# Kernel tuning notes

Measured on AMD Instinct MI355X. Metric: run time of the kernel, lower is better.

Reference implementation:

```python
import jax, jax.numpy as jnp
import numpy as np
import math

B, N, E, H = 2, 2048, 1024, 16
D = E // H

def setup_inputs() -> dict:
    key = jax.random.key(0)
    ks = jax.random.split(key, 9)
    s = 1.0 / math.sqrt(E)
    return {
        "x": jax.random.normal(ks[0], (B, N, E), dtype=jnp.float32),
        "Wq": jax.random.uniform(ks[1], (E, E), jnp.float32, -s, s),
        "bq": jax.random.uniform(ks[2], (E,), jnp.float32, -s, s),
        "Wk": jax.random.uniform(ks[3], (E, E), jnp.float32, -s, s),
        "bk": jax.random.uniform(ks[4], (E,), jnp.float32, -s, s),
        "Wv": jax.random.uniform(ks[5], (E, E), jnp.float32, -s, s),
        "bv": jax.random.uniform(ks[6], (E,), jnp.float32, -s, s),
        "Wo": jax.random.uniform(ks[7], (E, E), jnp.float32, -s, s),
        "bo": jax.random.uniform(ks[8], (E,), jnp.float32, -s, s),
    }

def _split_heads(t):
    # [b, n, (h d)] -> [b, h, n, d]
    b, n, _ = t.shape
    return t.reshape(b, n, H, D).transpose(0, 2, 1, 3)

def reference(x, Wq, bq, Wk, bk, Wv, bv, Wo, bo):
    q = _split_heads(x @ Wq.T + bq)
    k = _split_heads(x @ Wk.T + bk)
    v = _split_heads(x @ Wv.T + bv)
    energy = jnp.einsum('bhqd,bhkd->bhqk', q, k)
    # Faithful to source: softmax first, THEN divide by sqrt(n_embedding)
    attention = jax.nn.softmax(energy, axis=-1) / jnp.sqrt(jnp.float32(E))
    out = jnp.einsum('bhqk,bhkd->bhqd', attention, v)
    out = out.transpose(0, 2, 1, 3).reshape(x.shape[0], x.shape[1], E)
    return out @ Wo.T + bo
```

## Files before the change

kernel.cpp:

```cpp
#include <hip/hip_runtime.h>


typedef __bf16 bf16x8 __attribute__((ext_vector_type(8)));
typedef float  f32x4  __attribute__((ext_vector_type(4)));
typedef float  f32x16 __attribute__((ext_vector_type(16)));
using u16 = unsigned short;
using u32 = unsigned int;
typedef u16 u16x8 __attribute__((ext_vector_type(8)));
typedef u16 u16x4 __attribute__((ext_vector_type(4)));
typedef u32 u32x4 __attribute__((ext_vector_type(4)));

constexpr int BATCH = 2, SEQ = 2048, EMB = 1024, NH = 16, HD = 64;
constexpr int MTOT = BATCH * SEQ;
constexpr int KTOT = EMB;
constexpr int NTOT = EMB;
constexpr float LOG2E = 1.44269504088896340736f;
constexpr float FMAX2 = 32.0f;

constexpr size_t OFF_XBF = 0;
constexpr size_t OFF_WQ  = 8u * 1024 * 1024;
constexpr size_t OFF_WK  = OFF_WQ + 2u * 1024 * 1024;
constexpr size_t OFF_WV  = OFF_WK + 2u * 1024 * 1024;
constexpr size_t OFF_WO  = OFF_WV + 2u * 1024 * 1024;
constexpr size_t OFF_Q   = OFF_WO + 2u * 1024 * 1024;
constexpr size_t OFF_K   = OFF_Q  + 8u * 1024 * 1024;
constexpr size_t OFF_VT  = OFF_K  + 8u * 1024 * 1024;

__device__ __forceinline__ u16 f2bf(float f) {
  u32 u = __builtin_bit_cast(u32, f);
  u = (u + 0x7fffu + ((u >> 16) & 1u)) >> 16;
  return (u16)u;
}

__device__ __forceinline__ bf16x8 ld_bf16x8(const u16* p) {
  return __builtin_bit_cast(bf16x8, *(const u16x8*)p);
}

__device__ __forceinline__ float fexp2(float x) {
#if __has_builtin(__builtin_amdgcn_exp2f)
  return __builtin_amdgcn_exp2f(x);
#else
  return exp2f(x);
#endif
}

__device__ __forceinline__ u32 cvtpk(float lo, float hi_) {
  u32 r;
  asm("v_cvt_pk_bf16_f32 %0, %1, %2" : "=v"(r) : "v"(lo), "v"(hi_));
  return r;
}

__device__ __forceinline__ void stage16(const void* g, void* l) {
#if __has_builtin(__builtin_amdgcn_global_load_lds)
  __builtin_amdgcn_global_load_lds(
      (__attribute__((address_space(1))) void*)const_cast<void*>(g),
      (__attribute__((address_space(3))) void*)l, 16, 0, 0);
#else
  int lane = threadIdx.x & 63;
  uint4 v = *(const uint4*)g;
  *(uint4*)((char*)l + lane * 16) = v;
#endif
}

__global__ __launch_bounds__(256) void cvt_all(
    const float* __restrict__ x, const float* __restrict__ wq,
    const float* __restrict__ wk, const float* __restrict__ wv,
    const float* __restrict__ wo, u16* __restrict__ ox, u16* __restrict__ oq,
    u16* __restrict__ okk, u16* __restrict__ ov, u16* __restrict__ oo) {
  int id = blockIdx.x;
  const float* in;
  u16* out;
  int i;
  if (id < 4096) {
    in = x; out = ox; i = id * 256 + threadIdx.x;
  } else {
    int z = (id - 4096) >> 10, r = (id - 4096) & 1023;
    in = (z == 0) ? wq : (z == 1) ? wk : (z == 2) ? wv : wo;
    out = (z == 0) ? oq : (z == 1) ? okk : (z == 2) ? ov : oo;
    i = r * 256 + threadIdx.x;
  }
  float4 f = ((const float4*)in)[i];
  u32 lo = (u32)f2bf(f.x) | ((u32)f2bf(f.y) << 16);
  u32 hi = (u32)f2bf(f.z) | ((u32)f2bf(f.w) << 16);
  ((uint2*)out)[i] = make_uint2(lo, hi);
}

__device__ __forceinline__ void gemm_bt_core(const u16* __restrict__ A,
                                             const u16* __restrict__ Bm,
                                             const float* __restrict__ bias,
                                             void* __restrict__ out, int mode,
                                             float oscale) {
  __shared__ __align__(16) u16 smem[2][2][128 * 32];
  const int tid = threadIdx.x, w = tid >> 6, ln = tid & 63;
  const int wr = w >> 1, wc = w & 1, qq = ln >> 4, t = ln & 15;
  const int m0 = blockIdx.x * 128, n0 = blockIdx.y * 128;

  f32x4 acc[2][4] = {};

#define GSTAGE(bi, kt)                                                         \
  {                                                                            \
    int ck = w * 64 + ln;                                          \
    int r = ck >> 2, c2 = ck & 3;                                              \
    stage16(&A[(size_t)(m0 + r) * KTOT + (kt) + c2 * 8],                       \
            &smem[bi][0][(size_t)(w * 64) * 8]);                               \
    stage16(&Bm[(size_t)(n0 + r) * KTOT + (kt) + c2 * 8],                      \
            &smem[bi][1][(size_t)(w * 64) * 8]);                               \
  }

  GSTAGE(0, 0)
  __syncthreads();

  int bs = 0;
  for (int kt = 0; kt < KTOT; kt += 32, bs ^= 1) {
    if (kt + 32 < KTOT) GSTAGE(bs ^ 1, kt + 32)
    const u16* sA = smem[bs][0];
    const u16* sB = smem[bs][1];

    bf16x8 av[2], bv[4];
#pragma unroll
    for (int f = 0; f < 2; f++)
      av[f] = ld_bf16x8(&sA[(wr * 32 + f * 16 + t) * 32 + qq * 8]);
#pragma unroll
    for (int f = 0; f < 4; f++)
      bv[f] = ld_bf16x8(&sB[(wc * 64 + f * 16 + t) * 32 + qq * 8]);
#pragma unroll
    for (int i = 0; i < 2; i++)
#pragma unroll
      for (int j = 0; j < 4; j++)
        acc[i][j] = __builtin_amdgcn_mfma_f32_16x16x32_bf16(av[i], bv[j], acc[i][j], 0, 0, 0);
    __syncthreads();
  }
#undef GSTAGE

  if (mode == 1) {
    u16* tb = (u16*)smem;
    const int b = m0 >> 11;
    const int t16 = tid & 15;
    const int tokb = (m0 & 2047) + t16 * 8;
#pragma unroll
    for (int ph = 0; ph < 2; ph++) {
      if (ph == 1) __syncthreads();
      if (wc == ph) {
#pragma unroll
        for (int fc = 0; fc < 4; fc++) {
          int nl = fc * 16 + t;
          float bn = bias[n0 + ph * 64 + nl];
#pragma unroll
          for (int fr = 0; fr < 2; fr++)
#pragma unroll
            for (int i = 0; i < 4; i++) {
              int ml = wr * 32 + fr * 16 + qq * 4 + i;
              tb[nl * 128 + (ml ^ ((nl & 7) << 4))] = f2bf(acc[fr][fc][i] + bn);
            }
        }
      }
      __syncthreads();
#pragma unroll
      for (int p = 0; p < 2; p++) {
        int row = p * 32 + (tid >> 4);
        int n = n0 + ph * 64 + row;
        int hh = n >> 6, d = n & 63;
        u16x8 vd = *(const u16x8*)&tb[row * 128 + ((t16 * 8) ^ ((row & 7) << 4))];
        *(u16x8*)&((u16*)out)[(((size_t)(b * NH + hh)) * HD + d) * SEQ + tokb] = vd;
      }
    }
    return;
  }

#pragma unroll
  for (int fc = 0; fc < 4; fc++) {
    int n = n0 + wc * 64 + fc * 16 + t;
    float bn = bias[n];
#pragma unroll
    for (int fr = 0; fr < 2; fr++) {
#pragma unroll
      for (int i = 0; i < 4; i++) {
        int m = m0 + wr * 32 + fr * 16 + qq * 4 + i;
        float v = (acc[fr][fc][i] + bn) * oscale;
        if (mode == 2) {
          ((float*)out)[(size_t)m * NTOT + n] = v;
        } else {
          int b = m >> 11, tok = m & 2047, h = n >> 6, d = n & 63;
          ((u16*)out)[(((size_t)(b * NH + h)) * SEQ + tok) * HD + d] = f2bf(v);
        }
      }
    }
  }
}

__global__ __launch_bounds__(512) void gemm_qkv(
    const u16* __restrict__ A, const u16* __restrict__ WQ, const u16* __restrict__ WK,
    const u16* __restrict__ WV, const float* __restrict__ bq, const float* __restrict__ bk,
    const float* __restrict__ bv, u16* Qo, u16* Ko, u16* Vo) {
  int z = blockIdx.z;
  const u16* Bm = (z == 0) ? WQ : ((z == 1) ? WK : WV);
  const float* bias = (z == 0) ? bq : ((z == 1) ? bk : bv);
  u16* out = (z == 0) ? Qo : ((z == 1) ? Ko : Vo);
  gemm_bt_core(A, Bm, bias, out, (z == 2) ? 1 : 0, (z == 0) ? LOG2E : 1.0f);
}

__global__ __launch_bounds__(512) void gemm_o(const u16* __restrict__ A,
                                              const u16* __restrict__ WO,
                                              const float* __restrict__ bo,
                                              float* __restrict__ out) {
  gemm_bt_core(A, WO, bo, out, 2, 1.0f);
}

__global__ __launch_bounds__(512, 4) void flash_attn(const u16* __restrict__ Q,
                                                     const u16* __restrict__ Kg,
                                                     const u16* __restrict__ VT,
                                                     u16* __restrict__ O) {
  const int e = blockIdx.x;
  const int xcd = e & 7, slot = e >> 3;
  const int bh = xcd * 4 + (slot & 3);
  const int qt = slot >> 2;

  const int tid = threadIdx.x, w = tid >> 6, ln = tid & 63;
  const int c = ln & 31, hi = ln >> 5;
  const int kb = w >> 2;
  const int q0 = qt * 128 + (w & 3) * 32;

  const u16* Qb = Q + (size_t)bh * SEQ * HD;
  const u16* Kb = Kg + (size_t)bh * SEQ * HD;
  const u16* Vb = VT + (size_t)bh * HD * SEQ;

  __shared__ __align__(16) u16 sK[3][64 * 64];
  __shared__ __align__(16) u16 sV[3][64 * 64];
  __shared__ float sml[8][64];

  bf16x8 qf[4];
#pragma unroll
  for (int ks = 0; ks < 4; ks++)
    qf[ks] = ld_bf16x8(&Qb[(size_t)(q0 + c) * HD + ks * 16 + hi * 8]);

  f32x16 ot[2];
  ot[0] = 0.f; ot[1] = 0.f;
  float l = 0.f;

#define STAGE(pK, pV, kt)                                                      \
  {                                                                            \
    int ck = w * 64 + ln;                                                      \
    int r = ck >> 3, c2 = ck & 7, c2s = c2 ^ (r & 7);                          \
    stage16(&Kb[(size_t)((kt) + r) * HD + c2s * 8], (pK) + (size_t)(w * 64) * 8); \
    stage16(&Vb[(size_t)r * SEQ + (kt) + c2s * 8], (pV) + (size_t)(w * 64) * 8);  \
  }

#define QKT(stv, pK)                                                           \
  {                                                                            \
    stv = 0.f;                                                                 \
    __builtin_amdgcn_s_setprio(1);                                             \
    _Pragma("unroll") for (int ks = 0; ks < 4; ks++) {                         \
      int row = kb * 32 + c;                                                   \
      int boff = ((2 * ks + hi) ^ (row & 7)) << 4;                             \
      bf16x8 kf = ld_bf16x8((const u16*)((const char*)((pK) + row * 64) + boff)); \
      stv = __builtin_amdgcn_mfma_f32_32x32x16_bf16(kf, qf[ks], stv, 0, 0, 0); \
    }                                                                          \
    __builtin_amdgcn_s_setprio(0);                                             \
  }

#define SMAXPV(stv, pV)                                                        \
  {                                                                            \
    _Pragma("unroll") for (int i = 0; i < 16; i++)                             \
      stv[i] = fexp2(stv[i] - FMAX2);                                          \
    float u0 = (stv[0] + stv[1]) + (stv[2] + stv[3]);                          \
    float u1 = (stv[4] + stv[5]) + (stv[6] + stv[7]);                          \
    float u2 = (stv[8] + stv[9]) + (stv[10] + stv[11]);                        \
    float u3 = (stv[12] + stv[13]) + (stv[14] + stv[15]);                      \
    float rs = (u0 + u1) + (u2 + u3);                                          \
    l += rs + __shfl_xor(rs, 32);                                              \
    bf16x8 pb[2];                                                              \
    _Pragma("unroll") for (int ks2 = 0; ks2 < 2; ks2++) {                      \
      const int R0 = 8 * ks2;                                                  \
      const int R1 = 4 * ((2 * ks2 + 1) & 3);                                  \
      u32 X0 = cvtpk(stv[R0], stv[R0 + 1]);                                    \
      u32 X1 = cvtpk(stv[R0 + 2], stv[R0 + 3]);                                \
      u32 Y0 = cvtpk(stv[R1], stv[R1 + 1]);                                    \
      u32 Y1 = cvtpk(stv[R1 + 2], stv[R1 + 3]);                                \
      asm("v_permlane32_swap_b32 %0, %1" : "+v"(X0), "+v"(Y0));                \
      asm("v_permlane32_swap_b32 %0, %1" : "+v"(X1), "+v"(Y1));                \
      u32x4 wd; wd.x = X0; wd.y = X1; wd.z = Y0; wd.w = Y1;                    \
      pb[ks2] = __builtin_bit_cast(bf16x8, wd);                                \
    }                                                                          \
    __builtin_amdgcn_s_setprio(1);                                             \
    _Pragma("unroll") for (int ks2 = 0; ks2 < 2; ks2++) {                      \
      _Pragma("unroll") for (int db = 0; db < 2; db++) {                       \
        int row = db * 32 + c;                                                 \
        int boff = ((kb * 4 + ks2 * 2 + hi) ^ (row & 7)) << 4;                 \
        bf16x8 vf = ld_bf16x8((const u16*)((const char*)((pV) + row * 64) + boff)); \
        ot[db] = __builtin_amdgcn_mfma_f32_32x32x16_bf16(vf, pb[ks2], ot[db], 0, 0, 0); \
      }                                                                        \
    }                                                                          \
    __builtin_amdgcn_s_setprio(0);                                             \
  }

#define ROTATE()                                                               \
  { u16* x_ = kC; kC = kN; kN = kF; kF = x_;                                   \
    x_ = vC; vC = vN; vN = vF; vF = x_; }

  u16 *kC = sK[0], *kN = sK[1], *kF = sK[2];
  u16 *vC = sV[0], *vN = sV[1], *vF = sV[2];

  f32x16 stA, stB;

  STAGE(kC, vC, 0)
  __syncthreads();
  QKT(stA, kC)
  STAGE(kN, vN, 64)
  __syncthreads();

  for (int t = 0; t < 32; t += 2) {
    if (t + 2 < 32) STAGE(kF, vF, (t + 2) * 64)
    if (t + 1 < 32) QKT(stB, kN)
    SMAXPV(stA, vC)
    __syncthreads();
    ROTATE()
    if (t + 3 < 32) STAGE(kF, vF, (t + 3) * 64)
    if (t + 2 < 32) QKT(stA, kN)
    SMAXPV(stB, vC)
    __syncthreads();
    ROTATE()
  }
#undef STAGE
#undef QKT
#undef SMAXPV
#undef ROTATE

  float myl = l;
  const int pair = w & 3;
  float* xA = (float*)sK;
  float* xB = (float*)sV;
  {
    f32x16 give = (w < 4) ? ot[1] : ot[0];
    *(f32x16*)((w < 4 ? xA : xB) + (size_t)(pair * 64 + ln) * 16) = give;
    sml[w][ln] = myl;
  }
  __syncthreads();

  float po = sml[w ^ 4][ln];
  float lf = myl + po;
  float inv = 1.0f / (lf * 32.0f);
  f32x16 oth = *(const f32x16*)((w < 4 ? xB : xA) + (size_t)(pair * 64 + ln) * 16);
  f32x16 own = (w < 4) ? ot[0] : ot[1];
  const int db = (w < 4) ? 0 : 1;

  const int b = bh >> 4, h = bh & 15;
  u16* obase = O + ((size_t)(b * SEQ + q0 + c)) * EMB + h * HD;
#pragma unroll
  for (int g = 0; g < 4; g++) {
    u16x4 pkt;
#pragma unroll
    for (int i = 0; i < 4; i++)
      pkt[i] = f2bf((own[g * 4 + i] + oth[g * 4 + i]) * inv);
    *(u16x4*)(obase + db * 32 + g * 8 + hi * 4) = pkt;
  }
}

extern "C" void kernel_launch(void* const* d_in, const int* in_sizes, int n_in,
                              void* d_out, int out_size, void* d_ws, size_t ws_size,
                              hipStream_t stream) {
  const float* x  = (const float*)d_in[0];
  const float* Wq = (const float*)d_in[1];
  const float* bq = (const float*)d_in[2];
  const float* Wk = (const float*)d_in[3];
  const float* bk = (const float*)d_in[4];
  const float* Wv = (const float*)d_in[5];
  const float* bv = (const float*)d_in[6];
  const float* Wo = (const float*)d_in[7];
  const float* bo = (const float*)d_in[8];

  char* ws = (char*)d_ws;
  u16* xbf = (u16*)(ws + OFF_XBF);
  u16* wqb = (u16*)(ws + OFF_WQ);
  u16* wkb = (u16*)(ws + OFF_WK);
  u16* wvb = (u16*)(ws + OFF_WV);
  u16* wob = (u16*)(ws + OFF_WO);
  u16* Qw  = (u16*)(ws + OFF_Q);
  u16* Kw  = (u16*)(ws + OFF_K);
  u16* Vw  = (u16*)(ws + OFF_VT);

  cvt_all<<<dim3(8192), 256, 0, stream>>>(x, Wq, Wk, Wv, Wo, xbf, wqb, wkb, wvb, wob);

  gemm_qkv<<<dim3(MTOT / 128, NTOT / 128, 3), 512, 0, stream>>>(
      xbf, wqb, wkb, wvb, bq, bk, bv, Qw, Kw, Vw);

  flash_attn<<<dim3(512), 512, 0, stream>>>(Qw, Kw, Vw, xbf);

  gemm_o<<<dim3(MTOT / 128, NTOT / 128), 512, 0, stream>>>(xbf, wob, bo, (float*)d_out);
}
```

Baseline: 110.4 us.

## Give output projection its own 128x64-tile GEMM kernel with more blocks

```diff
diff --git a/kernel.cpp b/kernel.cpp
--- a/kernel.cpp
+++ b/kernel.cpp
@@ -177,12 +177,8 @@
       for (int i = 0; i < 4; i++) {
         int m = m0 + wr * 32 + fr * 16 + qq * 4 + i;
         float v = (acc[fr][fc][i] + bn) * oscale;
-        if (mode == 2) {
-          ((float*)out)[(size_t)m * NTOT + n] = v;
-        } else {
-          int b = m >> 11, tok = m & 2047, h = n >> 6, d = n & 63;
-          ((u16*)out)[(((size_t)(b * NH + h)) * SEQ + tok) * HD + d] = f2bf(v);
-        }
+        int b = m >> 11, tok = m & 2047, h = n >> 6, d = n & 63;
+        ((u16*)out)[(((size_t)(b * NH + h)) * SEQ + tok) * HD + d] = f2bf(v);
       }
     }
   }
@@ -203,7 +199,56 @@
                                               const u16* __restrict__ WO,
                                               const float* __restrict__ bo,
                                               float* __restrict__ out) {
-  gemm_bt_core(A, WO, bo, out, 2, 1.0f);
+  __shared__ __align__(16) u16 sA[2][128 * 32];
+  __shared__ __align__(16) u16 sB[2][64 * 32];
+  const int tid = threadIdx.x, w = tid >> 6, ln = tid & 63;
+  const int qq = ln >> 4, t = ln & 15;
+  const int m0 = blockIdx.x * 128, n0 = blockIdx.y * 64;
+
+  f32x4 acc[4] = {};
+
+#define OSTAGE(bi, kt)                                                         \
+  {                                                                            \
+    int ck = w * 64 + ln;                                          \
+    int rA = ck >> 2, cA = ck & 3;                                             \
+    stage16(&A[(size_t)(m0 + rA) * KTOT + (kt) + cA * 8],                      \
+            &sA[bi][(size_t)(w * 64) * 8]);                                    \
+    if (w < 4) {                                            \
+      int rB = ck >> 2, cB = ck & 3;                                           \
+      stage16(&WO[(size_t)(n0 + rB) * KTOT + (kt) + cB * 8],                   \
+              &sB[bi][(size_t)(w * 64) * 8]);                                  \
+    }                                                                          \
+  }
+
+  OSTAGE(0, 0)
+  __syncthreads();
+
+  int bs = 0;
+  for (int kt = 0; kt < KTOT; kt += 32, bs ^= 1) {
+    if (kt + 32 < KTOT) OSTAGE(bs ^ 1, kt + 32)
+
+    bf16x8 av = ld_bf16x8(&sA[bs][(w * 16 + t) * 32 + qq * 8]);
+    bf16x8 bv[4];
+#pragma unroll
+    for (int f = 0; f < 4; f++)
+      bv[f] = ld_bf16x8(&sB[bs][(f * 16 + t) * 32 + qq * 8]);
+#pragma unroll
+    for (int j = 0; j < 4; j++)
+      acc[j] = __builtin_amdgcn_mfma_f32_16x16x32_bf16(av, bv[j], acc[j], 0, 0, 0);
+    __syncthreads();
+  }
+#undef OSTAGE
+
+#pragma unroll
+  for (int fc = 0; fc < 4; fc++) {
+    int n = n0 + fc * 16 + t;
+    float bn = bo[n];
+#pragma unroll
+    for (int i = 0; i < 4; i++) {
+      int m = m0 + w * 16 + qq * 4 + i;
+      out[(size_t)m * NTOT + n] = acc[fc][i] + bn;
+    }
+  }
 }
 
 __global__ __launch_bounds__(512, 4) void flash_attn(const u16* __restrict__ Q,
@@ -385,5 +430,5 @@
 
   flash_attn<<<dim3(512), 512, 0, stream>>>(Qw, Kw, Vw, xbf);
 
-  gemm_o<<<dim3(MTOT / 128, NTOT / 128), 512, 0, stream>>>(xbf, wob, bo, (float*)d_out);
-}
+  gemm_o<<<dim3(MTOT / 128, NTOT / 64), 512, 0, stream>>>(xbf, wob, bo, (float*)d_out);
+}
```

Result: no change. 111.6 us (+1.0%).
